# Kernel tuning notes

Hardware: AMD Instinct MI355X
Metric: run time of the kernel (lower is better)

## Reference

```python
import jax, jax.numpy as jnp
import numpy as np

B, S, D, H = 2, 2048, 1024, 16
DH = D // H


def setup_inputs() -> dict:
    key = jax.random.key(0)
    ks = jax.random.split(key, 11)
    s = 0.02
    return {
        "queries": jax.random.normal(ks[0], (B, S, D), dtype=jnp.float32),
        "keys": jax.random.normal(ks[1], (B, S, D), dtype=jnp.float32),
        "values": jax.random.normal(ks[2], (B, S, D), dtype=jnp.float32),
        "Wq": jax.random.normal(ks[3], (D, D), dtype=jnp.float32) * s,
        "bq": jnp.zeros((D,), dtype=jnp.float32),
        "Wk": jax.random.normal(ks[4], (D, D), dtype=jnp.float32) * s,
        "bk": jnp.zeros((D,), dtype=jnp.float32),
        "Wv": jax.random.normal(ks[5], (D, D), dtype=jnp.float32) * s,
        "bv": jnp.zeros((D,), dtype=jnp.float32),
        "Wo": jax.random.normal(ks[6], (D, D), dtype=jnp.float32) * s,
        "bo": jnp.zeros((D,), dtype=jnp.float32),
    }


def _split_heads(x):
    # [B,S,D] -> [B,H,S,Dh]
    b, s, _ = x.shape
    return x.reshape(b, s, H, DH).transpose(0, 2, 1, 3)


def reference(queries, keys, values, Wq, bq, Wk, bk, Wv, bv, Wo, bo):
    q = _split_heads(queries @ Wq + bq)   # [B,H,S,Dh]
    k = _split_heads(keys @ Wk + bk)
    v = _split_heads(values @ Wv + bv)
    # d_k in the original is the last dim AFTER head split -> head_dim
    scale = 1.0 / jnp.sqrt(jnp.float32(DH))
    scores = jnp.einsum("bhqd,bhkd->bhqk", q, k) * scale  # [B,H,S,S]
    weights = jax.nn.softmax(scores, axis=-1)
    o = jnp.einsum("bhqk,bhkd->bhqd", weights, v)         # [B,H,S,Dh]
    o = o.transpose(0, 2, 1, 3).reshape(queries.shape[0], queries.shape[1], D)
    return o @ Wo + bo
```

## Files before the change

kernel.cpp:

```cpp
#include <hip/hip_runtime.h>
#include <stdint.h>

#define B_ 2
#define S_ 2048
#define D_ 1024
#define H_ 16
#define DH_ 64
#define M_ 4096

typedef unsigned short u16;
typedef unsigned int u32;
typedef short mfma_elem_t;
typedef mfma_elem_t bfrag8 __attribute__((ext_vector_type(8)));
typedef float floatx4 __attribute__((ext_vector_type(4)));

__device__ __forceinline__ u16 f2bf(float f) {
  unsigned u = __float_as_uint(f);
  u += 0x7fff + ((u >> 16) & 1);
  return (u16)(u >> 16);
}

__device__ __forceinline__ u32 pack_bf16(float a, float b) {
  u32 ua = __float_as_uint(a) + 0x8000u;
  u32 ub = __float_as_uint(b) + 0x8000u;
#if __has_builtin(__builtin_amdgcn_perm)
  return __builtin_amdgcn_perm(ub, ua, 0x07060302u);
#else
  return (ua >> 16) | (ub & 0xffff0000u);
#endif
}

__device__ __forceinline__ void gl_lds16(const void* g, void* l) {
  __builtin_amdgcn_global_load_lds(
      (__attribute__((address_space(1))) void*)(g),
      (__attribute__((address_space(3))) void*)(l), 16, 0, 0);
}

__global__ __launch_bounds__(256) void k_convert_x(
    const float* __restrict__ q, const float* __restrict__ k, const float* __restrict__ v,
    u16* __restrict__ xq, u16* __restrict__ xk, u16* __restrict__ xv) {
  const float* src = blockIdx.z == 0 ? q : (blockIdx.z == 1 ? k : v);
  u16* dst = blockIdx.z == 0 ? xq : (blockIdx.z == 1 ? xk : xv);
  int i = (blockIdx.x * 256 + threadIdx.x) * 4;
  float4 f = *(const float4*)(src + i);
  ushort4 o;
  o.x = f2bf(f.x); o.y = f2bf(f.y); o.z = f2bf(f.z); o.w = f2bf(f.w);
  *(ushort4*)(dst + i) = o;
}

__global__ __launch_bounds__(256) void k_convert_w(
    const float* __restrict__ wq, const float* __restrict__ wk,
    const float* __restrict__ wv, const float* __restrict__ wo,
    u16* __restrict__ tq, u16* __restrict__ tk, u16* __restrict__ tv, u16* __restrict__ to_) {
  const int gz = blockIdx.z;
  const float* w = gz == 0 ? wq : gz == 1 ? wk : gz == 2 ? wv : wo;
  u16* t = gz == 0 ? tq : gz == 1 ? tk : gz == 2 ? tv : to_;
  __shared__ float tile[32][33];
  int r0 = blockIdx.y * 32, c0 = blockIdx.x * 32;
  int tx = threadIdx.x, ty = threadIdx.y;
#pragma unroll
  for (int i = 0; i < 4; i++) {
    int r = ty + i * 8;
    tile[r][tx] = w[(size_t)(r0 + r) * D_ + c0 + tx];
  }
  __syncthreads();
#pragma unroll
  for (int i = 0; i < 4; i++) {
    int r = ty + i * 8;
    t[(size_t)(c0 + r) * D_ + r0 + tx] = f2bf(tile[tx][r]);
  }
}

__global__ __launch_bounds__(256, 3) void k_gemm_qkv(
    const u16* __restrict__ xq, const u16* __restrict__ xk, const u16* __restrict__ xv,
    const u16* __restrict__ wtq, const u16* __restrict__ wtk, const u16* __restrict__ wtv,
    const float* __restrict__ bq, const float* __restrict__ bk, const float* __restrict__ bv,
    u16* __restrict__ oq, u16* __restrict__ ok, u16* __restrict__ ovt) {
  const int gz = blockIdx.z;
  const u16* X = gz == 0 ? xq : gz == 1 ? xk : xv;
  const u16* WT = gz == 0 ? wtq : gz == 1 ? wtk : wtv;
  const float* bias = gz == 0 ? bq : gz == 1 ? bk : bv;
  u16* outsd = gz == 0 ? oq : ok;

  __shared__ u16 sbuf[2][8192];

  const int t = threadIdx.x;
  const int w = t >> 6, lane = t & 63, l15 = lane & 15, quad = lane >> 4;
  const int wm = (w >> 1) * 64, wn = (w & 1) * 64;
  const int m0 = blockIdx.y * 128, n0 = blockIdx.x * 128;

  floatx4 acc[4][4];
  floatx4 zero = {0.f, 0.f, 0.f, 0.f};
#pragma unroll
  for (int mt = 0; mt < 4; mt++)
#pragma unroll
    for (int nt = 0; nt < 4; nt++) acc[mt][nt] = zero;

  auto stage = [&](int kt, int b) {
    int k0 = kt * 32;
#pragma unroll
    for (int i = 0; i < 2; i++) {
      int chunk = i * 256 + t;
      gl_lds16(X + (size_t)(m0 + (chunk >> 2)) * D_ + k0 + (chunk & 3) * 8,
               sbuf[b] + i * 2048 + w * 512);
      gl_lds16(WT + (size_t)(n0 + (chunk >> 2)) * D_ + k0 + (chunk & 3) * 8,
               sbuf[b] + 4096 + i * 2048 + w * 512);
    }
  };

  stage(0, 0);
  for (int kt = 0; kt < 32; kt++) {
    __syncthreads();
    if (kt < 31) stage(kt + 1, (kt + 1) & 1);
    const u16* As = sbuf[kt & 1];
    const u16* Bs = sbuf[kt & 1] + 4096;
    bfrag8 af[4], bf[4];
#pragma unroll
    for (int mt = 0; mt < 4; mt++)
      af[mt] = *(const bfrag8*)(As + (wm + mt * 16 + l15) * 32 + quad * 8);
#pragma unroll
    for (int nt = 0; nt < 4; nt++)
      bf[nt] = *(const bfrag8*)(Bs + (wn + nt * 16 + l15) * 32 + quad * 8);
#pragma unroll
    for (int mt = 0; mt < 4; mt++)
#pragma unroll
      for (int nt = 0; nt < 4; nt++)
        acc[mt][nt] = __builtin_amdgcn_mfma_f32_16x16x32_bf16(af[mt], bf[nt], acc[mt][nt], 0, 0, 0);
  }

  if (gz < 2) {
#pragma unroll
    for (int mt = 0; mt < 4; mt++)
#pragma unroll
      for (int nt = 0; nt < 4; nt++) {
        int Nc = n0 + wn + nt * 16 + l15;
        float bv_ = bias[Nc];
        int hh = Nc >> 6, dh = Nc & 63;
#pragma unroll
        for (int r = 0; r < 4; r++) {
          int Mr = m0 + wm + mt * 16 + quad * 4 + r;
          int bb = Mr >> 11, ss = Mr & 2047;
          outsd[((size_t)(bb * H_ + hh) * S_ + ss) * DH_ + dh] = f2bf(acc[mt][nt][r] + bv_);
        }
      }
  } else {
#pragma unroll
    for (int mt = 0; mt < 4; mt++)
#pragma unroll
      for (int nt = 0; nt < 4; nt++) {
        int Nc = n0 + wn + nt * 16 + l15;
        float bv_ = bias[Nc];
        int hh = Nc >> 6, dh = Nc & 63;
        int Mr0 = m0 + wm + mt * 16 + quad * 4;
        int bb = Mr0 >> 11, ss0 = Mr0 & 2047;
        ushort4 o;
        o.x = f2bf(acc[mt][nt][0] + bv_);
        o.y = f2bf(acc[mt][nt][1] + bv_);
        o.z = f2bf(acc[mt][nt][2] + bv_);
        o.w = f2bf(acc[mt][nt][3] + bv_);
        *(ushort4*)(ovt + ((size_t)(bb * H_ + hh) * DH_ + dh) * S_ + ss0) = o;
      }
  }
}

__global__ __launch_bounds__(256, 3) void k_gemm_final(
    const u16* __restrict__ X, const u16* __restrict__ WT,
    const float* __restrict__ bias, float* __restrict__ out) {
  __shared__ u16 sbuf[2][8192];
  const int t = threadIdx.x;
  const int w = t >> 6, lane = t & 63, l15 = lane & 15, quad = lane >> 4;
  const int wm = (w >> 1) * 64, wn = (w & 1) * 64;
  const int m0 = blockIdx.y * 128, n0 = blockIdx.x * 128;

  floatx4 acc[4][4];
  floatx4 zero = {0.f, 0.f, 0.f, 0.f};
#pragma unroll
  for (int mt = 0; mt < 4; mt++)
#pragma unroll
    for (int nt = 0; nt < 4; nt++) acc[mt][nt] = zero;

  auto stage = [&](int kt, int b) {
    int k0 = kt * 32;
#pragma unroll
    for (int i = 0; i < 2; i++) {
      int chunk = i * 256 + t;
      gl_lds16(X + (size_t)(m0 + (chunk >> 2)) * D_ + k0 + (chunk & 3) * 8,
               sbuf[b] + i * 2048 + w * 512);
      gl_lds16(WT + (size_t)(n0 + (chunk >> 2)) * D_ + k0 + (chunk & 3) * 8,
               sbuf[b] + 4096 + i * 2048 + w * 512);
    }
  };

  stage(0, 0);
  for (int kt = 0; kt < 32; kt++) {
    __syncthreads();
    if (kt < 31) stage(kt + 1, (kt + 1) & 1);
    const u16* As = sbuf[kt & 1];
    const u16* Bs = sbuf[kt & 1] + 4096;
    bfrag8 af[4], bf[4];
#pragma unroll
    for (int mt = 0; mt < 4; mt++)
      af[mt] = *(const bfrag8*)(As + (wm + mt * 16 + l15) * 32 + quad * 8);
#pragma unroll
    for (int nt = 0; nt < 4; nt++)
      bf[nt] = *(const bfrag8*)(Bs + (wn + nt * 16 + l15) * 32 + quad * 8);
#pragma unroll
    for (int mt = 0; mt < 4; mt++)
#pragma unroll
      for (int nt = 0; nt < 4; nt++)
        acc[mt][nt] = __builtin_amdgcn_mfma_f32_16x16x32_bf16(af[mt], bf[nt], acc[mt][nt], 0, 0, 0);
  }
#pragma unroll
  for (int mt = 0; mt < 4; mt++)
#pragma unroll
    for (int nt = 0; nt < 4; nt++) {
      int Nc = n0 + wn + nt * 16 + l15;
      float bv_ = bias[Nc];
#pragma unroll
      for (int r = 0; r < 4; r++) {
        int Mr = m0 + wm + mt * 16 + quad * 4 + r;
        out[(size_t)Mr * D_ + Nc] = acc[mt][nt][r] + bv_;
      }
    }
}

__global__ __launch_bounds__(256, 2) void k_attn(
    const u16* __restrict__ Q, const u16* __restrict__ K,
    const u16* __restrict__ Vt, u16* __restrict__ O) {
  __shared__ u16 lds[25600];

  const int t = threadIdx.x, w = t >> 6, lane = t & 63, l15 = lane & 15, quad = lane >> 4;
  const int bh = blockIdx.z * H_ + blockIdx.y;
  const int q0 = blockIdx.x * 128;
  const u16* Qb = Q + (size_t)bh * S_ * DH_;
  const u16* Kb = K + (size_t)bh * S_ * DH_;
  const u16* Vb = Vt + (size_t)bh * DH_ * S_;
  u16* Pw = lds + 16384 + w * 2304;

  bfrag8 qf[2][2];
#pragma unroll
  for (int mt = 0; mt < 2; mt++)
#pragma unroll
    for (int ks = 0; ks < 2; ks++)
      qf[mt][ks] = *(const bfrag8*)(Qb + (size_t)(q0 + w * 32 + mt * 16 + l15) * DH_ + ks * 32 + quad * 8);

  auto stage = [&](int kv0, int b) {
    u16* Kbuf = lds + b * 8192;
    u16* Vbuf = lds + b * 8192 + 4096;
#pragma unroll
    for (int ks = 0; ks < 2; ks++)
      gl_lds16(Kb + (size_t)(kv0 + (t >> 2)) * DH_ + ks * 32 + (t & 3) * 8,
               Kbuf + ks * 2048 + w * 512);
#pragma unroll
    for (int ksp = 0; ksp < 2; ksp++)
      gl_lds16(Vb + (size_t)(t >> 2) * S_ + kv0 + ksp * 32 + (t & 3) * 8,
               Vbuf + ksp * 2048 + w * 512);
  };

  floatx4 oacc[2][4];
  float lrow[2] = {0.f, 0.f};
  floatx4 zero = {0.f, 0.f, 0.f, 0.f};
#pragma unroll
  for (int mt = 0; mt < 2; mt++)
#pragma unroll
    for (int dt = 0; dt < 4; dt++) oacc[mt][dt] = zero;
  const float cexp = 0.125f * 1.4426950408889634f;

  stage(0, 0);
  for (int kt = 0; kt < 32; kt++) {
    __syncthreads();
    if (kt < 31) stage((kt + 1) * 64, (kt + 1) & 1);
    const u16* Kbuf = lds + (kt & 1) * 8192;
    const u16* Vbuf = lds + (kt & 1) * 8192 + 4096;

    floatx4 sacc[2][4];
#pragma unroll
    for (int mt = 0; mt < 2; mt++)
#pragma unroll
      for (int nt = 0; nt < 4; nt++) sacc[mt][nt] = zero;
#pragma unroll
    for (int nt = 0; nt < 4; nt++) {
      bfrag8 kf0 = *(const bfrag8*)(Kbuf + (nt * 16 + l15) * 32 + quad * 8);
      bfrag8 kf1 = *(const bfrag8*)(Kbuf + 2048 + (nt * 16 + l15) * 32 + quad * 8);
      sacc[0][nt] = __builtin_amdgcn_mfma_f32_16x16x32_bf16(kf0, qf[0][0], sacc[0][nt], 0, 0, 0);
      sacc[0][nt] = __builtin_amdgcn_mfma_f32_16x16x32_bf16(kf1, qf[0][1], sacc[0][nt], 0, 0, 0);
      sacc[1][nt] = __builtin_amdgcn_mfma_f32_16x16x32_bf16(kf0, qf[1][0], sacc[1][nt], 0, 0, 0);
      sacc[1][nt] = __builtin_amdgcn_mfma_f32_16x16x32_bf16(kf1, qf[1][1], sacc[1][nt], 0, 0, 0);
    }

#pragma unroll
    for (int mt = 0; mt < 2; mt++) {
#pragma unroll
      for (int nt = 0; nt < 4; nt++) {
        float p0 = __builtin_amdgcn_exp2f(sacc[mt][nt][0] * cexp);
        float p1 = __builtin_amdgcn_exp2f(sacc[mt][nt][1] * cexp);
        float p2 = __builtin_amdgcn_exp2f(sacc[mt][nt][2] * cexp);
        float p3 = __builtin_amdgcn_exp2f(sacc[mt][nt][3] * cexp);
        lrow[mt] += (p0 + p1) + (p2 + p3);
        uint2 pd;
        pd.x = pack_bf16(p0, p1);
        pd.y = pack_bf16(p2, p3);
        *(uint2*)(Pw + (mt * 16 + l15) * 72 + nt * 16 + quad * 4) = pd;
      }
    }

#pragma unroll
    for (int ksp = 0; ksp < 2; ksp++) {
      bfrag8 pf0 = *(const bfrag8*)(Pw + (0 + l15) * 72 + ksp * 32 + quad * 8);
      bfrag8 pf1 = *(const bfrag8*)(Pw + (16 + l15) * 72 + ksp * 32 + quad * 8);
#pragma unroll
      for (int dt = 0; dt < 4; dt++) {
        bfrag8 vf = *(const bfrag8*)(Vbuf + ksp * 2048 + (dt * 16 + l15) * 32 + quad * 8);
        oacc[0][dt] = __builtin_amdgcn_mfma_f32_16x16x32_bf16(vf, pf0, oacc[0][dt], 0, 0, 0);
        oacc[1][dt] = __builtin_amdgcn_mfma_f32_16x16x32_bf16(vf, pf1, oacc[1][dt], 0, 0, 0);
      }
    }
  }

#pragma unroll
  for (int mt = 0; mt < 2; mt++) {
    float l = lrow[mt];
    l += __shfl_xor(l, 16, 64);
    l += __shfl_xor(l, 32, 64);
    float rinv = 1.0f / l;
    int qrow = q0 + w * 32 + mt * 16 + l15;
#pragma unroll
    for (int dt = 0; dt < 4; dt++) {
      ushort4 o;
      o.x = f2bf(oacc[mt][dt][0] * rinv);
      o.y = f2bf(oacc[mt][dt][1] * rinv);
      o.z = f2bf(oacc[mt][dt][2] * rinv);
      o.w = f2bf(oacc[mt][dt][3] * rinv);
      *(ushort4*)(O + ((size_t)blockIdx.z * S_ + qrow) * D_ + blockIdx.y * DH_ + dt * 16 + quad * 4) = o;
    }
  }
}

extern "C" void kernel_launch(void* const* d_in, const int* in_sizes, int n_in,
                              void* d_out, int out_size, void* d_ws, size_t ws_size,
                              hipStream_t stream) {
  const float* queries = (const float*)d_in[0];
  const float* keys = (const float*)d_in[1];
  const float* values = (const float*)d_in[2];
  const float* Wq = (const float*)d_in[3];
  const float* bq = (const float*)d_in[4];
  const float* Wk = (const float*)d_in[5];
  const float* bk = (const float*)d_in[6];
  const float* Wv = (const float*)d_in[7];
  const float* bv = (const float*)d_in[8];
  const float* Wo = (const float*)d_in[9];
  const float* bo = (const float*)d_in[10];

  const size_t NXB = (size_t)M_ * D_ * 2;
  const size_t WB = (size_t)D_ * D_ * 2;
  if (ws_size < 7 * NXB + 4 * WB) return;

  char* ws = (char*)d_ws;
  u16* Xq = (u16*)(ws);
  u16* Xk = (u16*)(ws + NXB);
  u16* Xv = (u16*)(ws + 2 * NXB);
  u16* WqT = (u16*)(ws + 3 * NXB);
  u16* WkT = (u16*)(ws + 3 * NXB + WB);
  u16* WvT = (u16*)(ws + 3 * NXB + 2 * WB);
  u16* WoT = (u16*)(ws + 3 * NXB + 3 * WB);
  char* ws2 = ws + 3 * NXB + 4 * WB;
  u16* Qhs = (u16*)(ws2);
  u16* Khs = (u16*)(ws2 + NXB);
  u16* VtB = (u16*)(ws2 + 2 * NXB);
  u16* Obuf = (u16*)(ws2 + 3 * NXB);
  float* outp = (float*)d_out;

  k_convert_x<<<dim3(4096, 1, 3), 256, 0, stream>>>(queries, keys, values, Xq, Xk, Xv);
  k_convert_w<<<dim3(32, 32, 4), dim3(32, 8), 0, stream>>>(Wq, Wk, Wv, Wo, WqT, WkT, WvT, WoT);
  k_gemm_qkv<<<dim3(8, 32, 3), 256, 0, stream>>>(Xq, Xk, Xv, WqT, WkT, WvT, bq, bk, bv, Qhs, Khs, VtB);
  k_attn<<<dim3(16, 16, 2), 256, 0, stream>>>(Qhs, Khs, VtB, Obuf);
  k_gemm_final<<<dim3(8, 32), 256, 0, stream>>>(Obuf, WoT, bo, outp);
}
```

Baseline: 227.2 us.

## Split attention KV tile across wave pairs and fold softmax scale into Q projection

Each wave now handles 64 query rows and half of a 128-wide KV tile, so K/V fragments loaded from LDS are reused across four query tiles. The two partial outputs are combined through LDS at the end. The softmax scale times log2(e) is folded into the Q projection epilogue, removing a multiply per score. Double buffering is dropped in favour of a single 128-key stage with two barriers per iteration, which exposes global-load latency in exchange for fewer iterations and higher register use.

```diff
diff --git a/kernel.cpp b/kernel.cpp
--- a/kernel.cpp
+++ b/kernel.cpp
@@ -81,6 +81,7 @@
   const u16* WT = gz == 0 ? wtq : gz == 1 ? wtk : wtv;
   const float* bias = gz == 0 ? bq : gz == 1 ? bk : bv;
   u16* outsd = gz == 0 ? oq : ok;
+  const float qscale = gz == 0 ? 0.125f * 1.4426950408889634f : 1.0f;
 
   __shared__ u16 sbuf[2][8192];
 
@@ -140,7 +141,8 @@
         for (int r = 0; r < 4; r++) {
           int Mr = m0 + wm + mt * 16 + quad * 4 + r;
           int bb = Mr >> 11, ss = Mr & 2047;
-          outsd[((size_t)(bb * H_ + hh) * S_ + ss) * DH_ + dh] = f2bf(acc[mt][nt][r] + bv_);
+          outsd[((size_t)(bb * H_ + hh) * S_ + ss) * DH_ + dh] =
+              f2bf((acc[mt][nt][r] + bv_) * qscale);
         }
       }
   } else {
@@ -232,106 +234,124 @@
   const int t = threadIdx.x, w = t >> 6, lane = t & 63, l15 = lane & 15, quad = lane >> 4;
   const int bh = blockIdx.z * H_ + blockIdx.y;
   const int q0 = blockIdx.x * 128;
+  const int qh = (w >> 1) * 64;
+  const int kh = (w & 1) * 64;
   const u16* Qb = Q + (size_t)bh * S_ * DH_;
   const u16* Kb = K + (size_t)bh * S_ * DH_;
   const u16* Vb = Vt + (size_t)bh * DH_ * S_;
   u16* Pw = lds + 16384 + w * 2304;
 
-  bfrag8 qf[2][2];
-#pragma unroll
-  for (int mt = 0; mt < 2; mt++)
+  bfrag8 qf[4][2];
+#pragma unroll
+  for (int qt = 0; qt < 4; qt++)
 #pragma unroll
     for (int ks = 0; ks < 2; ks++)
-      qf[mt][ks] = *(const bfrag8*)(Qb + (size_t)(q0 + w * 32 + mt * 16 + l15) * DH_ + ks * 32 + quad * 8);
-
-  auto stage = [&](int kv0, int b) {
-    u16* Kbuf = lds + b * 8192;
-    u16* Vbuf = lds + b * 8192 + 4096;
-#pragma unroll
-    for (int ks = 0; ks < 2; ks++)
-      gl_lds16(Kb + (size_t)(kv0 + (t >> 2)) * DH_ + ks * 32 + (t & 3) * 8,
-               Kbuf + ks * 2048 + w * 512);
-#pragma unroll
-    for (int ksp = 0; ksp < 2; ksp++)
-      gl_lds16(Vb + (size_t)(t >> 2) * S_ + kv0 + ksp * 32 + (t & 3) * 8,
-               Vbuf + ksp * 2048 + w * 512);
-  };
-
-  floatx4 oacc[2][4];
-  float lrow[2] = {0.f, 0.f};
+      qf[qt][ks] = *(const bfrag8*)(Qb + (size_t)(q0 + qh + qt * 16 + l15) * DH_ + ks * 32 + quad * 8);
+
+  floatx4 oacc[4][4];
+  float lrow[4] = {0.f, 0.f, 0.f, 0.f};
   floatx4 zero = {0.f, 0.f, 0.f, 0.f};
 #pragma unroll
-  for (int mt = 0; mt < 2; mt++)
-#pragma unroll
-    for (int dt = 0; dt < 4; dt++) oacc[mt][dt] = zero;
-  const float cexp = 0.125f * 1.4426950408889634f;
-
-  stage(0, 0);
-  for (int kt = 0; kt < 32; kt++) {
+  for (int qt = 0; qt < 4; qt++)
+#pragma unroll
+    for (int dt = 0; dt < 4; dt++) oacc[qt][dt] = zero;
+
+  for (int kt = 0; kt < 16; kt++) {
+    const int kv0 = kt * 128;
+#pragma unroll
+    for (int i = 0; i < 4; i++) {
+      int chunk = i * 256 + t;
+      gl_lds16(Kb + (size_t)(kv0 + ((chunk >> 2) & 127)) * DH_ + (chunk >> 9) * 32 + (chunk & 3) * 8,
+               lds + i * 2048 + w * 512);
+      gl_lds16(Vb + (size_t)(t >> 2) * S_ + kv0 + i * 32 + (t & 3) * 8,
+               lds + 8192 + i * 2048 + w * 512);
+    }
     __syncthreads();
-    if (kt < 31) stage((kt + 1) * 64, (kt + 1) & 1);
-    const u16* Kbuf = lds + (kt & 1) * 8192;
-    const u16* Vbuf = lds + (kt & 1) * 8192 + 4096;
-
-    floatx4 sacc[2][4];
-#pragma unroll
-    for (int mt = 0; mt < 2; mt++)
-#pragma unroll
-      for (int nt = 0; nt < 4; nt++) sacc[mt][nt] = zero;
+
+    floatx4 sacc[4][4];
 #pragma unroll
     for (int nt = 0; nt < 4; nt++) {
-      bfrag8 kf0 = *(const bfrag8*)(Kbuf + (nt * 16 + l15) * 32 + quad * 8);
-      bfrag8 kf1 = *(const bfrag8*)(Kbuf + 2048 + (nt * 16 + l15) * 32 + quad * 8);
-      sacc[0][nt] = __builtin_amdgcn_mfma_f32_16x16x32_bf16(kf0, qf[0][0], sacc[0][nt], 0, 0, 0);
-      sacc[0][nt] = __builtin_amdgcn_mfma_f32_16x16x32_bf16(kf1, qf[0][1], sacc[0][nt], 0, 0, 0);
-      sacc[1][nt] = __builtin_amdgcn_mfma_f32_16x16x32_bf16(kf0, qf[1][0], sacc[1][nt], 0, 0, 0);
-      sacc[1][nt] = __builtin_amdgcn_mfma_f32_16x16x32_bf16(kf1, qf[1][1], sacc[1][nt], 0, 0, 0);
-    }
-
-#pragma unroll
-    for (int mt = 0; mt < 2; mt++) {
-#pragma unroll
-      for (int nt = 0; nt < 4; nt++) {
-        float p0 = __builtin_amdgcn_exp2f(sacc[mt][nt][0] * cexp);
-        float p1 = __builtin_amdgcn_exp2f(sacc[mt][nt][1] * cexp);
-        float p2 = __builtin_amdgcn_exp2f(sacc[mt][nt][2] * cexp);
-        float p3 = __builtin_amdgcn_exp2f(sacc[mt][nt][3] * cexp);
-        lrow[mt] += (p0 + p1) + (p2 + p3);
-        uint2 pd;
-        pd.x = pack_bf16(p0, p1);
-        pd.y = pack_bf16(p2, p3);
-        *(uint2*)(Pw + (mt * 16 + l15) * 72 + nt * 16 + quad * 4) = pd;
-      }
-    }
-
-#pragma unroll
-    for (int ksp = 0; ksp < 2; ksp++) {
-      bfrag8 pf0 = *(const bfrag8*)(Pw + (0 + l15) * 72 + ksp * 32 + quad * 8);
-      bfrag8 pf1 = *(const bfrag8*)(Pw + (16 + l15) * 72 + ksp * 32 + quad * 8);
+      bfrag8 kf0 = *(const bfrag8*)(lds + (kh + nt * 16 + l15) * 32 + quad * 8);
+      bfrag8 kf1 = *(const bfrag8*)(lds + 4096 + (kh + nt * 16 + l15) * 32 + quad * 8);
+#pragma unroll
+      for (int qt = 0; qt < 4; qt++) {
+        floatx4 s0 = __builtin_amdgcn_mfma_f32_16x16x32_bf16(kf0, qf[qt][0], zero, 0, 0, 0);
+        sacc[nt][qt] = __builtin_amdgcn_mfma_f32_16x16x32_bf16(kf1, qf[qt][1], s0, 0, 0, 0);
+      }
+    }
+
+#pragma unroll
+    for (int c = 0; c < 2; c++) {
+#pragma unroll
+      for (int j = 0; j < 2; j++) {
+        const int nt = c * 2 + j;
+#pragma unroll
+        for (int qt = 0; qt < 4; qt++) {
+          float p0 = __builtin_amdgcn_exp2f(sacc[nt][qt][0]);
+          float p1 = __builtin_amdgcn_exp2f(sacc[nt][qt][1]);
+          float p2 = __builtin_amdgcn_exp2f(sacc[nt][qt][2]);
+          float p3 = __builtin_amdgcn_exp2f(sacc[nt][qt][3]);
+          lrow[qt] += (p0 + p1) + (p2 + p3);
+          uint2 pd;
+          pd.x = pack_bf16(p0, p1);
+          pd.y = pack_bf16(p2, p3);
+          *(uint2*)(Pw + (qt * 16 + l15) * 36 + j * 16 + quad * 4) = pd;
+        }
+      }
+      bfrag8 pf[4];
+#pragma unroll
+      for (int qt = 0; qt < 4; qt++)
+        pf[qt] = *(const bfrag8*)(Pw + (qt * 16 + l15) * 36 + quad * 8);
 #pragma unroll
       for (int dt = 0; dt < 4; dt++) {
-        bfrag8 vf = *(const bfrag8*)(Vbuf + ksp * 2048 + (dt * 16 + l15) * 32 + quad * 8);
-        oacc[0][dt] = __builtin_amdgcn_mfma_f32_16x16x32_bf16(vf, pf0, oacc[0][dt], 0, 0, 0);
-        oacc[1][dt] = __builtin_amdgcn_mfma_f32_16x16x32_bf16(vf, pf1, oacc[1][dt], 0, 0, 0);
-      }
-    }
-  }
-
-#pragma unroll
-  for (int mt = 0; mt < 2; mt++) {
-    float l = lrow[mt];
+        bfrag8 vf = *(const bfrag8*)(lds + 8192 + ((w & 1) * 2 + c) * 2048 + (dt * 16 + l15) * 32 + quad * 8);
+#pragma unroll
+        for (int qt = 0; qt < 4; qt++)
+          oacc[qt][dt] = __builtin_amdgcn_mfma_f32_16x16x32_bf16(vf, pf[qt], oacc[qt][dt], 0, 0, 0);
+      }
+    }
+    __syncthreads();
+  }
+
+  float* ocmb = (float*)lds;
+  float* lcmb = (float*)lds + 8704;
+  const int p = w >> 1;
+
+#pragma unroll
+  for (int qt = 0; qt < 4; qt++) {
+    float l = lrow[qt];
     l += __shfl_xor(l, 16, 64);
     l += __shfl_xor(l, 32, 64);
-    float rinv = 1.0f / l;
-    int qrow = q0 + w * 32 + mt * 16 + l15;
-#pragma unroll
-    for (int dt = 0; dt < 4; dt++) {
-      ushort4 o;
-      o.x = f2bf(oacc[mt][dt][0] * rinv);
-      o.y = f2bf(oacc[mt][dt][1] * rinv);
-      o.z = f2bf(oacc[mt][dt][2] * rinv);
-      o.w = f2bf(oacc[mt][dt][3] * rinv);
-      *(ushort4*)(O + ((size_t)blockIdx.z * S_ + qrow) * D_ + blockIdx.y * DH_ + dt * 16 + quad * 4) = o;
+    lrow[qt] = l;
+  }
+
+  if (w & 1) {
+    float* po = ocmb + p * 4352;
+#pragma unroll
+    for (int qt = 0; qt < 4; qt++) {
+#pragma unroll
+      for (int dt = 0; dt < 4; dt++)
+        *(floatx4*)(po + (qt * 16 + l15) * 68 + dt * 16 + quad * 4) = oacc[qt][dt];
+      if (quad == 0) lcmb[p * 64 + qt * 16 + l15] = lrow[qt];
+    }
+  }
+  __syncthreads();
+  if (!(w & 1)) {
+    float* po = ocmb + p * 4352;
+#pragma unroll
+    for (int qt = 0; qt < 4; qt++) {
+      float rinv = 1.0f / (lrow[qt] + lcmb[p * 64 + qt * 16 + l15]);
+      int qrow = q0 + qh + qt * 16 + l15;
+#pragma unroll
+      for (int dt = 0; dt < 4; dt++) {
+        floatx4 oo = oacc[qt][dt] + *(const floatx4*)(po + (qt * 16 + l15) * 68 + dt * 16 + quad * 4);
+        ushort4 o;
+        o.x = f2bf(oo[0] * rinv);
+        o.y = f2bf(oo[1] * rinv);
+        o.z = f2bf(oo[2] * rinv);
+        o.w = f2bf(oo[3] * rinv);
+        *(ushort4*)(O + ((size_t)blockIdx.z * S_ + qrow) * D_ + blockIdx.y * DH_ + dt * 16 + quad * 4) = o;
+      }
     }
   }
 }
```

New measurement: 238.4 us. 4.9% more time.
